# Performance work log

Hardware: AMD Instinct MI355X
Metric: run time of the kernel (lower is better)

The kernel has to match this reference:

```python
import jax, jax.numpy as jnp
import numpy as np

B = 1048576  # batch size
EPS_CLAMP_LO = 1e-6
EPS_CLAMP_HI = 1.0 - 1e-6


def _build_mask():
    # mask[k, i, j] = 1 iff i + j == k, flattened to [19, 100]
    i = np.arange(10)
    m = np.zeros((19, 10, 10), dtype=np.float32)
    ii, jj = np.meshgrid(i, i, indexing='ij')
    m[(ii + jj).ravel(), ii.ravel(), jj.ravel()] = 1.0
    return jnp.asarray(m.reshape(19, 100))


def setup_inputs() -> dict:
    key = jax.random.key(0)
    k1, k2, k3, k4 = jax.random.split(key, 4)
    # concept probabilities: uniform then normalize rows to sum 1
    p1 = jax.random.uniform(k1, (B, 10), dtype=jnp.float32)
    p1 = p1 / p1.sum(axis=1, keepdims=True)
    p2 = jax.random.uniform(k2, (B, 10), dtype=jnp.float32)
    p2 = p2 / p2.sum(axis=1, keepdims=True)
    # learnable permutation-tree weights (binaryTreeLogicNet leaf maps)
    W1 = jax.random.uniform(k3, (10, 10), dtype=jnp.float32)
    W2 = jax.random.uniform(k4, (10, 10), dtype=jnp.float32)
    mask = _build_mask()
    return {"p1": p1, "p2": p2, "W1": W1, "W2": W2, "mask": mask}


def _minmax_norm(W):
    lo = W.min(axis=1, keepdims=True)
    hi = W.max(axis=1, keepdims=True)
    return (W - lo) / (hi - lo + 1e-8)


def reference(p1, p2, W1, W2, mask):
    # input_to_leaf: learned soft permutation with minmax-normalized weights
    p1p = p1 @ _minmax_norm(W1)                      # [B,10]
    p2p = p2 @ _minmax_norm(W2)                      # [B,10]
    # MinMaxAggregator graded AND at andness=1.0 -> elementwise min over all pairs
    s = jnp.minimum(p1p[:, :, None], p2p[:, None, :])  # [B,10,10]
    one_minus = 1.0 - jnp.clip(s, EPS_CLAMP_LO, EPS_CLAMP_HI)
    log_one_minus = jnp.log(one_minus + 1e-12).reshape(-1, 100)  # [B,100]
    # fused masked reduction over all 19 sum bins: [B,100] @ [100,19]
    log_prod = log_one_minus @ mask.T                # [B,19]
    y_prob = 1.0 - jnp.exp(log_prod)                 # smooth OR per sum class
    y_prob = y_prob / (y_prob.sum(axis=1, keepdims=True) + 1e-9)
    return y_prob
```

## Files before the change

### kernel.cpp

```cpp
#include <hip/hip_runtime.h>


#define NBLOCKS 1024
#define PANELS 4

__global__ __launch_bounds__(256, 4) void bacon_main(
    const float* __restrict__ p1, const float* __restrict__ p2,
    const float* __restrict__ W1, const float* __restrict__ W2,
    float* __restrict__ out)
{
    __shared__ __align__(16) float s_out[2][4864];
    __shared__ __align__(16) float s_w[240];

    const int t = threadIdx.x;
    const int blk = blockIdx.x;
    const size_t row0 = (size_t)blk * (256 * PANELS) + t;

    float2 va[2][5], vb[2][5];
    {
        const float2* g1 = (const float2*)(p1 + row0 * 10);
        const float2* g2 = (const float2*)(p2 + row0 * 10);
        #pragma unroll
        for (int e = 0; e < 5; ++e) { va[0][e] = g1[e]; vb[0][e] = g2[e]; }
    }

    if (t < 20) {
        const float* row = ((t < 10) ? W1 : W2) + (t % 10) * 10;
        float r[10];
        #pragma unroll
        for (int i = 0; i < 10; ++i) r[i] = row[i];
        float lo = r[0], hi = r[0];
        #pragma unroll
        for (int i = 1; i < 10; ++i) {
            lo = fminf(lo, r[i]);
            hi = fmaxf(hi, r[i]);
        }
        float inv = 1.0f / (hi - lo + 1e-8f);
        float* o = s_w + ((t < 10) ? 0 : 120) + (t % 10) * 12;
        #pragma unroll
        for (int i = 0; i < 10; ++i) o[i] = (r[i] - lo) * inv;
        o[10] = 0.0f; o[11] = 0.0f;
    }
    __syncthreads();

    #pragma unroll
    for (int p = 0; p < PANELS; ++p) {
        const int cur = p & 1;

        if (p + 1 < PANELS) {
            const int nxt = cur ^ 1;
            const float2* g1 = (const float2*)(p1 + (row0 + (size_t)(p + 1) * 256) * 10);
            const float2* g2 = (const float2*)(p2 + (row0 + (size_t)(p + 1) * 256) * 10);
            #pragma unroll
            for (int e = 0; e < 5; ++e) { va[nxt][e] = g1[e]; vb[nxt][e] = g2[e]; }
        }

        float A[10], Bv[10];
        #pragma unroll
        for (int i = 0; i < 10; ++i) { A[i] = 1.0f; Bv[i] = 1.0f; }
        #pragma unroll
        for (int k = 0; k < 10; ++k) {
            const float ak = (k & 1) ? va[cur][k >> 1].y : va[cur][k >> 1].x;
            const float bk = (k & 1) ? vb[cur][k >> 1].y : vb[cur][k >> 1].x;
            const float4* w1q = (const float4*)(s_w + k * 12);
            const float4* w2q = (const float4*)(s_w + 120 + k * 12);
            float4 u0 = w1q[0], u1 = w1q[1];
            float2 u2 = *(const float2*)(s_w + k * 12 + 8);
            float4 v0 = w2q[0], v1 = w2q[1];
            float2 v2 = *(const float2*)(s_w + 120 + k * 12 + 8);
            A[0] = fmaf(-ak, u0.x, A[0]); A[1] = fmaf(-ak, u0.y, A[1]);
            A[2] = fmaf(-ak, u0.z, A[2]); A[3] = fmaf(-ak, u0.w, A[3]);
            A[4] = fmaf(-ak, u1.x, A[4]); A[5] = fmaf(-ak, u1.y, A[5]);
            A[6] = fmaf(-ak, u1.z, A[6]); A[7] = fmaf(-ak, u1.w, A[7]);
            A[8] = fmaf(-ak, u2.x, A[8]); A[9] = fmaf(-ak, u2.y, A[9]);
            Bv[0] = fmaf(-bk, v0.x, Bv[0]); Bv[1] = fmaf(-bk, v0.y, Bv[1]);
            Bv[2] = fmaf(-bk, v0.z, Bv[2]); Bv[3] = fmaf(-bk, v0.w, Bv[3]);
            Bv[4] = fmaf(-bk, v1.x, Bv[4]); Bv[5] = fmaf(-bk, v1.y, Bv[5]);
            Bv[6] = fmaf(-bk, v1.z, Bv[6]); Bv[7] = fmaf(-bk, v1.w, Bv[7]);
            Bv[8] = fmaf(-bk, v2.x, Bv[8]); Bv[9] = fmaf(-bk, v2.y, Bv[9]);
        }

        float prod[19];
        #pragma unroll
        for (int k = 0; k < 19; ++k) prod[k] = 1.0f;
        #pragma unroll
        for (int i = 0; i < 10; ++i) {
            #pragma unroll
            for (int j = 0; j < 10; ++j) {
                prod[i + j] *= fmaxf(A[i], Bv[j]);
            }
        }

        float y[19];
        float tot = 0.0f;
        #pragma unroll
        for (int k = 0; k < 19; ++k) { y[k] = 1.0f - prod[k]; tot += y[k]; }
        float invn = __builtin_amdgcn_rcpf(tot + 1e-9f);

        #pragma unroll
        for (int k = 0; k < 19; ++k) s_out[cur][t * 19 + k] = y[k] * invn;
        __syncthreads();

        {
            const float4* so = (const float4*)s_out[cur];
            float4* go = (float4*)(out + ((size_t)blk * PANELS + p) * 4864);
            #pragma unroll
            for (int it = 0; it < 5; ++it) {
                int idx = t + it * 256;
                if (idx < 1216) go[idx] = so[idx];
            }
        }
    }
}

extern "C" void kernel_launch(void* const* d_in, const int* in_sizes, int n_in,
                              void* d_out, int out_size, void* d_ws, size_t ws_size,
                              hipStream_t stream) {
    const float* p1 = (const float*)d_in[0];
    const float* p2 = (const float*)d_in[1];
    const float* W1 = (const float*)d_in[2];
    const float* W2 = (const float*)d_in[3];
    bacon_main<<<NBLOCKS, 256, 0, stream>>>(p1, p2, W1, W2, (float*)d_out);
}
```

Measured before the change: 154.0 us.

## Load all rows upfront and compute leaf maps with packed fp32 FMA

Replaces the double-buffered panel loop with loads of all four rows' inputs at kernel start, then computes the 10x10 leaf matmuls for all rows together using 2-wide vector FMAs (packed fp32) while reusing the weight loads from shared memory across rows. Launch bounds drop from 4 to 2 waves per SIMD target to allow the larger register footprint. This aims to cut FMA instruction count and shared-memory weight reads, and to raise memory-level parallelism. The cost is higher register pressure and lower occupancy.

```diff
diff --git a/kernel.cpp b/kernel.cpp
--- a/kernel.cpp
+++ b/kernel.cpp
@@ -1,10 +1,12 @@
 #include <hip/hip_runtime.h>
 
 
+typedef float v2f __attribute__((ext_vector_type(2)));
+
 #define NBLOCKS 1024
-#define PANELS 4
+#define ROWS 4
 
-__global__ __launch_bounds__(256, 4) void bacon_main(
+__global__ __launch_bounds__(256, 2) void bacon_main(
     const float* __restrict__ p1, const float* __restrict__ p2,
     const float* __restrict__ W1, const float* __restrict__ W2,
     float* __restrict__ out)
@@ -14,14 +16,15 @@
 
     const int t = threadIdx.x;
     const int blk = blockIdx.x;
-    const size_t row0 = (size_t)blk * (256 * PANELS) + t;
+    const size_t base = (size_t)blk * (256 * ROWS);
 
-    float2 va[2][5], vb[2][5];
-    {
-        const float2* g1 = (const float2*)(p1 + row0 * 10);
-        const float2* g2 = (const float2*)(p2 + row0 * 10);
+    float2 va[ROWS][5], vb[ROWS][5];
+    #pragma unroll
+    for (int r = 0; r < ROWS; ++r) {
+        const float2* g1 = (const float2*)(p1 + (base + (size_t)r * 256 + t) * 10);
+        const float2* g2 = (const float2*)(p2 + (base + (size_t)r * 256 + t) * 10);
         #pragma unroll
-        for (int e = 0; e < 5; ++e) { va[0][e] = g1[e]; vb[0][e] = g2[e]; }
+        for (int e = 0; e < 5; ++e) { va[r][e] = g1[e]; vb[r][e] = g2[e]; }
     }
 
     if (t < 20) {
@@ -43,41 +46,43 @@
     }
     __syncthreads();
 
+    v2f A2[ROWS][5], B2[ROWS][5];
     #pragma unroll
-    for (int p = 0; p < PANELS; ++p) {
-        const int cur = p & 1;
+    for (int r = 0; r < ROWS; ++r)
+        #pragma unroll
+        for (int m = 0; m < 5; ++m) { A2[r][m] = (v2f){1.0f, 1.0f}; B2[r][m] = (v2f){1.0f, 1.0f}; }
 
-        if (p + 1 < PANELS) {
-            const int nxt = cur ^ 1;
-            const float2* g1 = (const float2*)(p1 + (row0 + (size_t)(p + 1) * 256) * 10);
-            const float2* g2 = (const float2*)(p2 + (row0 + (size_t)(p + 1) * 256) * 10);
+    #pragma unroll
+    for (int k = 0; k < 10; ++k) {
+        const float4* w1q = (const float4*)(s_w + k * 12);
+        const float4* w2q = (const float4*)(s_w + 120 + k * 12);
+        float4 u0 = w1q[0], u1 = w1q[1];
+        float2 u2 = *(const float2*)(s_w + k * 12 + 8);
+        float4 v0 = w2q[0], v1 = w2q[1];
+        float2 v2 = *(const float2*)(s_w + 120 + k * 12 + 8);
+        v2f uw[5] = { {u0.x, u0.y}, {u0.z, u0.w}, {u1.x, u1.y}, {u1.z, u1.w}, {u2.x, u2.y} };
+        v2f vw[5] = { {v0.x, v0.y}, {v0.z, v0.w}, {v1.x, v1.y}, {v1.z, v1.w}, {v2.x, v2.y} };
+        #pragma unroll
+        for (int r = 0; r < ROWS; ++r) {
+            const float ak = (k & 1) ? va[r][k >> 1].y : va[r][k >> 1].x;
+            const float bk = (k & 1) ? vb[r][k >> 1].y : vb[r][k >> 1].x;
+            const v2f na = (v2f){-ak, -ak};
+            const v2f nb = (v2f){-bk, -bk};
             #pragma unroll
-            for (int e = 0; e < 5; ++e) { va[nxt][e] = g1[e]; vb[nxt][e] = g2[e]; }
+            for (int m = 0; m < 5; ++m) {
+                A2[r][m] = __builtin_elementwise_fma(na, uw[m], A2[r][m]);
+                B2[r][m] = __builtin_elementwise_fma(nb, vw[m], B2[r][m]);
+            }
         }
+    }
 
+    #pragma unroll
+    for (int r = 0; r < ROWS; ++r) {
         float A[10], Bv[10];
         #pragma unroll
-        for (int i = 0; i < 10; ++i) { A[i] = 1.0f; Bv[i] = 1.0f; }
-        #pragma unroll
-        for (int k = 0; k < 10; ++k) {
-            const float ak = (k & 1) ? va[cur][k >> 1].y : va[cur][k >> 1].x;
-            const float bk = (k & 1) ? vb[cur][k >> 1].y : vb[cur][k >> 1].x;
-            const float4* w1q = (const float4*)(s_w + k * 12);
-            const float4* w2q = (const float4*)(s_w + 120 + k * 12);
-            float4 u0 = w1q[0], u1 = w1q[1];
-            float2 u2 = *(const float2*)(s_w + k * 12 + 8);
-            float4 v0 = w2q[0], v1 = w2q[1];
-            float2 v2 = *(const float2*)(s_w + 120 + k * 12 + 8);
-            A[0] = fmaf(-ak, u0.x, A[0]); A[1] = fmaf(-ak, u0.y, A[1]);
-            A[2] = fmaf(-ak, u0.z, A[2]); A[3] = fmaf(-ak, u0.w, A[3]);
-            A[4] = fmaf(-ak, u1.x, A[4]); A[5] = fmaf(-ak, u1.y, A[5]);
-            A[6] = fmaf(-ak, u1.z, A[6]); A[7] = fmaf(-ak, u1.w, A[7]);
-            A[8] = fmaf(-ak, u2.x, A[8]); A[9] = fmaf(-ak, u2.y, A[9]);
-            Bv[0] = fmaf(-bk, v0.x, Bv[0]); Bv[1] = fmaf(-bk, v0.y, Bv[1]);
-            Bv[2] = fmaf(-bk, v0.z, Bv[2]); Bv[3] = fmaf(-bk, v0.w, Bv[3]);
-            Bv[4] = fmaf(-bk, v1.x, Bv[4]); Bv[5] = fmaf(-bk, v1.y, Bv[5]);
-            Bv[6] = fmaf(-bk, v1.z, Bv[6]); Bv[7] = fmaf(-bk, v1.w, Bv[7]);
-            Bv[8] = fmaf(-bk, v2.x, Bv[8]); Bv[9] = fmaf(-bk, v2.y, Bv[9]);
+        for (int m = 0; m < 5; ++m) {
+            A[2 * m] = A2[r][m].x;  A[2 * m + 1] = A2[r][m].y;
+            Bv[2 * m] = B2[r][m].x; Bv[2 * m + 1] = B2[r][m].y;
         }
 
         float prod[19];
@@ -97,13 +102,14 @@
         for (int k = 0; k < 19; ++k) { y[k] = 1.0f - prod[k]; tot += y[k]; }
         float invn = __builtin_amdgcn_rcpf(tot + 1e-9f);
 
+        const int cur = r & 1;
         #pragma unroll
         for (int k = 0; k < 19; ++k) s_out[cur][t * 19 + k] = y[k] * invn;
         __syncthreads();
 
         {
             const float4* so = (const float4*)s_out[cur];
-            float4* go = (float4*)(out + ((size_t)blk * PANELS + p) * 4864);
+            float4* go = (float4*)(out + ((size_t)blk * ROWS + r) * 4864);
             #pragma unroll
             for (int it = 0; it < 5; ++it) {
                 int idx = t + it * 256;
```

Measured after the change: 216.9 us. 40.9% more time.
